# Optimization experiments

Measured on AMD Instinct MI355X. Metric: run time of the kernel, lower is better.

The kernel has to match this reference:

```python
import jax, jax.numpy as jnp
import numpy as np

N_NODES = 65536
N_EDGES = 524288
N_GRAPHS = 512
G_NODES = 10000
NUM_DISEASES = 2000
IN_DIM = 128
HID = 256  # 2 * IN_DIM (z_emb concat feat)
D_FEAT = 512
C_FEAT = 512
MAX_Z = 4000


def setup_inputs() -> dict:
    key = jax.random.key(0)
    ks = jax.random.split(key, 20)
    rn = lambda k, shape: jax.random.normal(k, shape, dtype=jnp.float32) * 0.05
    return {
        "z": jax.random.randint(ks[0], (N_NODES,), 0, MAX_Z),
        "node_id": jnp.sort(jax.random.randint(ks[1], (N_NODES,), 0, G_NODES)),
        "src": jax.random.randint(ks[2], (N_EDGES,), 0, N_NODES),
        "dst": jax.random.randint(ks[3], (N_EDGES,), 0, N_NODES),
        "graph_ids": jnp.sort(jax.random.randint(ks[4], (N_NODES,), 0, N_GRAPHS)),
        "z_table": rn(ks[5], (MAX_Z, IN_DIM)),
        "d_feat_tab": rn(ks[6], (G_NODES, D_FEAT)),
        "c_feat_tab": rn(ks[7], (G_NODES, C_FEAT)),
        "Wd": rn(ks[8], (D_FEAT, IN_DIM)),
        "Wc": rn(ks[9], (C_FEAT, IN_DIM)),
        "gin_W1": rn(ks[10], (HID, HID)), "gin_b1": jnp.zeros((HID,), jnp.float32),
        "gin_W2": rn(ks[11], (HID, HID)), "gin_b2": jnp.zeros((HID,), jnp.float32),
        "sage_Wself": rn(ks[12], (HID, HID)),
        "sage_Wneigh": rn(ks[13], (HID, HID)),
        "sage_b": jnp.zeros((HID,), jnp.float32),
        "lin1_W": rn(ks[14], (HID, HID)), "lin1_b": jnp.zeros((HID,), jnp.float32),
        "lin2_W": rn(ks[15], (HID, 1)), "lin2_b": jnp.zeros((1,), jnp.float32),
    }


def reference(z, node_id, src, dst, graph_ids, z_table, d_feat_tab, c_feat_tab,
              Wd, Wc, gin_W1, gin_b1, gin_W2, gin_b2,
              sage_Wself, sage_Wneigh, sage_b, lin1_W, lin1_b, lin2_W, lin2_b):
    # --- input feature construction (Model.forward) ---
    z_emb = z_table[z]                               # [N, IN_DIM]
    d_proj = d_feat_tab[node_id] @ Wd                # d_fc (bias=False)
    c_proj = c_feat_tab[node_id] @ Wc                # c_fc (bias=False)
    disease = (node_id <= NUM_DISEASES)[:, None]
    # node_id is sorted -> masked concat order == node order
    feat = jnp.where(disease, d_proj, c_proj)        # [N, IN_DIM]
    x = jnp.concatenate([z_emb, feat], axis=1)       # [N, HID]
    # --- GINConv: sum aggregation, eps=0, mlp = Lin->ReLU->Lin ---
    agg = jax.ops.segment_sum(x[src], dst, num_segments=N_NODES)
    h = x + agg
    h = jax.nn.relu(h @ gin_W1 + gin_b1) @ gin_W2 + gin_b2
    # --- SAGEConv('mean'): fc_self(h) + fc_neigh(mean_neighbors) + bias ---
    deg = jax.ops.segment_sum(jnp.ones((N_EDGES,), h.dtype), dst, num_segments=N_NODES)
    mean_n = jax.ops.segment_sum(h[src], dst, num_segments=N_NODES) / jnp.maximum(deg, 1.0)[:, None]
    h = h @ sage_Wself + mean_n @ sage_Wneigh + sage_b
    # --- per-graph max pooling readout ---
    g = jax.ops.segment_max(h, graph_ids, num_segments=N_GRAPHS, indices_are_sorted=True)
    g = jnp.where(jnp.isfinite(g), g, 0.0)           # guard empty graphs
    # --- head: Linear -> ReLU -> (dropout p=0, eval) -> Linear ---
    h = jax.nn.relu(g @ lin1_W + lin1_b)
    return h @ lin2_W + lin2_b                       # [N_GRAPHS, 1]
```

## Files before the change

### kernel.cpp

```cpp
#include <hip/hip_runtime.h>
#include <hip/hip_bf16.h>

#define N_NODES     65536
#define N_EDGES     524288
#define N_GRAPHS    512
#define G_NODES_N   10000
#define NUM_DIS     2000
#define IN_DIM      128
#define HID         256
#define D_FEAT      512
#define MAX_Z       4000
#define POOL_SPLIT  8

typedef _Float16 half8 __attribute__((ext_vector_type(8)));
typedef float    f32x4 __attribute__((ext_vector_type(4)));

typedef __attribute__((address_space(1))) const void as1_void;
typedef __attribute__((address_space(3))) void       as3_void;

__global__ __launch_bounds__(256) void prep_kernel(
    const float* __restrict__ Ws, const float* __restrict__ Wn,
    const float* __restrict__ Wd, const float* __restrict__ Wc,
    const float* __restrict__ W1, const float* __restrict__ W2,
    const float* __restrict__ z_table,
    const int* __restrict__ z, const int* __restrict__ node_id,
    _Float16* __restrict__ WsT, _Float16* __restrict__ WnT,
    _Float16* __restrict__ WdT, _Float16* __restrict__ WcT,
    _Float16* __restrict__ W12P, _Float16* __restrict__ zt16,
    int2* __restrict__ zn2, int* __restrict__ cnt, int* __restrict__ flags)
{
    const int b = blockIdx.x;
    const int tid = threadIdx.x;
    if (b < 64) {
        __shared__ float tile[64][65];
        const float* W; _Float16* T; int K, N, k0, n0;
        if (b < 32) {
            const int mat = b >> 4, t = b & 15;
            K = HID; N = HID; k0 = (t >> 2) * 64; n0 = (t & 3) * 64;
            W = (mat == 0) ? Ws : Wn;
            T = (mat == 0) ? WsT : WnT;
        } else {
            const int bb = b - 32;
            const int mat = bb >> 4, t = bb & 15;
            K = D_FEAT; N = IN_DIM; k0 = (t >> 1) * 64; n0 = (t & 1) * 64;
            W = (mat == 0) ? Wd : Wc;
            T = (mat == 0) ? WdT : WcT;
        }
        const int tx = tid & 63, ty = tid >> 6;
        #pragma unroll
        for (int r = 0; r < 64; r += 4)
            tile[r + ty][tx] = W[(size_t)(k0 + r + ty) * N + n0 + tx];
        __syncthreads();
        #pragma unroll
        for (int c = 0; c < 64; c += 4)
            T[(size_t)(n0 + c + ty) * K + k0 + tx] = (_Float16)tile[tx][c + ty];
    } else if (b < 576) {
        const int bb = b - 64;
        const int mat = bb >> 8;
        const int k = bb & 255;
        const int n = tid;
        const float* W = mat ? W2 : W1;
        const float v = W[(size_t)k * HID + n];
        const size_t idx = (size_t)(mat * 8 + (k >> 5)) * 8192
                         + (size_t)((((k >> 3) & 3) * 256 + n) * 8 + (k & 7));
        W12P[idx] = (_Float16)v;
    } else if (b < 826) {
        const size_t base = ((size_t)(b - 576) * 256 + tid) * 8;
        const float4 f0 = *(const float4*)(z_table + base);
        const float4 f1 = *(const float4*)(z_table + base + 4);
        half8 h;
        h[0]=(_Float16)f0.x; h[1]=(_Float16)f0.y; h[2]=(_Float16)f0.z; h[3]=(_Float16)f0.w;
        h[4]=(_Float16)f1.x; h[5]=(_Float16)f1.y; h[6]=(_Float16)f1.z; h[7]=(_Float16)f1.w;
        *(half8*)(zt16 + base) = h;
    } else if (b < 890) {
        const int base = (b - 826) * 1024 + tid * 4;
        *(int4*)(cnt + base) = make_int4(0, 0, 0, 0);
        if (b == 826 && tid < 128) flags[tid] = 0;
    } else {
        const int i = (b - 890) * 256 + tid;
        zn2[i] = make_int2(z[i], node_id[i]);
    }
}

__global__ __launch_bounds__(256) void proj_mfma_kernel(
    const float* __restrict__ dtab, const float* __restrict__ ctab,
    const _Float16* __restrict__ WdT, const _Float16* __restrict__ WcT,
    _Float16* __restrict__ proj)
{
    __shared__ _Float16 Alds[128 * 40];
    __shared__ _Float16 Blds[128 * 40];
    const int blk = blockIdx.x;
    const float* tab; const _Float16* WT; int base, M, bm;
    if (blk < 16) { tab = dtab; WT = WdT; base = 0;           M = NUM_DIS + 1;             bm = blk * 128; }
    else          { tab = ctab; WT = WcT; base = NUM_DIS + 1; M = G_NODES_N - NUM_DIS - 1; bm = (blk - 16) * 128; }
    const int tid  = threadIdx.x;
    const int wave = tid >> 6, lane = tid & 63;
    const int q    = lane >> 4, l16 = lane & 15;
    const int mbase = (wave & 1) * 64, nbase = (wave >> 1) * 64;
    const int r = tid >> 1, s = tid & 1;

    f32x4 acc[4][4] = {};

    for (int kc = 0; kc < 16; ++kc) {
        const int k0 = kc * 32;
        const int arow = min(bm + r, M - 1);
        const float* gA = tab + (size_t)(base + arow) * D_FEAT + k0 + s * 16;
        const _Float16* gB = WT + (size_t)r * D_FEAT + k0 + s * 16;
        const float4 f0 = ((const float4*)gA)[0];
        const float4 f1 = ((const float4*)gA)[1];
        const float4 f2 = ((const float4*)gA)[2];
        const float4 f3 = ((const float4*)gA)[3];
        const half8 hb0 = *(const half8*)gB;
        const half8 hb1 = *(const half8*)(gB + 8);
        half8 h0, h1;
        h0[0]=(_Float16)f0.x; h0[1]=(_Float16)f0.y; h0[2]=(_Float16)f0.z; h0[3]=(_Float16)f0.w;
        h0[4]=(_Float16)f1.x; h0[5]=(_Float16)f1.y; h0[6]=(_Float16)f1.z; h0[7]=(_Float16)f1.w;
        h1[0]=(_Float16)f2.x; h1[1]=(_Float16)f2.y; h1[2]=(_Float16)f2.z; h1[3]=(_Float16)f2.w;
        h1[4]=(_Float16)f3.x; h1[5]=(_Float16)f3.y; h1[6]=(_Float16)f3.z; h1[7]=(_Float16)f3.w;
        __syncthreads();
        *(half8*)&Alds[r * 40 + s * 16]     = h0;
        *(half8*)&Alds[r * 40 + s * 16 + 8] = h1;
        *(half8*)&Blds[r * 40 + s * 16]     = hb0;
        *(half8*)&Blds[r * 40 + s * 16 + 8] = hb1;
        __syncthreads();
        half8 a[4], b[4];
        #pragma unroll
        for (int i = 0; i < 4; ++i)
            a[i] = *(const half8*)&Alds[(mbase + i * 16 + l16) * 40 + q * 8];
        #pragma unroll
        for (int j = 0; j < 4; ++j)
            b[j] = *(const half8*)&Blds[(nbase + j * 16 + l16) * 40 + q * 8];
        #pragma unroll
        for (int i = 0; i < 4; ++i)
            #pragma unroll
            for (int j = 0; j < 4; ++j)
                acc[i][j] = __builtin_amdgcn_mfma_f32_16x16x32_f16(a[i], b[j], acc[i][j], 0, 0, 0);
    }

    #pragma unroll
    for (int j = 0; j < 4; ++j) {
        const int colg = nbase + j * 16 + l16;
        #pragma unroll
        for (int i = 0; i < 4; ++i) {
            #pragma unroll
            for (int rr = 0; rr < 4; ++rr) {
                const int row = bm + mbase + i * 16 + q * 4 + rr;
                if (row < M)
                    proj[(size_t)(base + row) * IN_DIM + colg] = (_Float16)acc[i][j][rr];
            }
        }
    }
}

__global__ __launch_bounds__(256) void hist_kernel(
    const int* __restrict__ dst, int* __restrict__ cnt)
{
    const int e = blockIdx.x * 256 + threadIdx.x;
    if (e < N_EDGES) atomicAdd(&cnt[dst[e]], 1);
}

__global__ __launch_bounds__(256) void scan_fused_kernel(
    const int* __restrict__ cnt, int* __restrict__ row_ptr,
    int* __restrict__ fill, int* __restrict__ flags)
{
    __shared__ int a[256], b[256];
    __shared__ int sums[64];
    __shared__ int segbase;
    const int t = threadIdx.x;
    const int blk = blockIdx.x;
    const int base = blk * 1024 + t * 4;
    const int4 c = *(const int4*)(cnt + base);
    const int s = c.x + c.y + c.z + c.w;
    a[t] = s;
    __syncthreads();
    int* in = a; int* out = b;
    for (int off = 1; off < 256; off <<= 1) {
        out[t] = in[t] + ((t >= off) ? in[t - off] : 0);
        __syncthreads();
        int* tmp = in; in = out; out = tmp;
    }
    if (t == 0) {
        atomicExch(&flags[64 + blk], in[255]);
        __threadfence();
        atomicAdd(&flags[0], 1);
        while (atomicAdd(&flags[0], 0) < 64) {}
    }
    __syncthreads();
    if (t < 64) sums[t] = atomicAdd(&flags[64 + t], 0);
    __syncthreads();
    if (t == 0) {
        int pfx = 0;
        for (int i = 0; i < blk; ++i) pfx += sums[i];
        segbase = pfx;
        if (blk == 63) {
            int tot = pfx;
            for (int i = blk; i < 64; ++i) tot += sums[i];
            row_ptr[N_NODES] = tot;
        }
    }
    __syncthreads();
    const int run = in[t] - s + segbase;
    int4 r;
    r.x = run; r.y = run + c.x; r.z = r.y + c.y; r.w = r.z + c.z;
    *(int4*)(row_ptr + base) = r;
    *(int4*)(fill + base) = r;
}

__global__ __launch_bounds__(256) void scatter_kernel(
    const int* __restrict__ src, const int* __restrict__ dst,
    const int2* __restrict__ zn2,
    int* __restrict__ fill, int* __restrict__ col, int2* __restrict__ colzn)
{
    const int e = blockIdx.x * 256 + threadIdx.x;
    if (e < N_EDGES) {
        const int s = src[e];
        const int pos = atomicAdd(&fill[dst[e]], 1);
        col[pos] = s;
        colzn[pos] = zn2[s];
    }
}

__global__ __launch_bounds__(256) void gin_fused_kernel(
    const int* __restrict__ row_ptr, const int2* __restrict__ colzn,
    const int2* __restrict__ zn2,
    const _Float16* __restrict__ zt16, const _Float16* __restrict__ proj,
    const _Float16* __restrict__ W12P,
    const float* __restrict__ b1, const float* __restrict__ b2,
    _Float16* __restrict__ H)
{
    __shared__ _Float16 Apanel[32 * 264];
    __shared__ _Float16 Blds[2][8192];

    const int bm   = blockIdx.x * 32;
    const int tid  = threadIdx.x;
    const int wave = tid >> 6, lane = tid & 63;
    const int q    = lane >> 4, l16 = lane & 15;
    const int nbase = wave * 64;

    auto stage = [&](int c, int buf) {
        const _Float16* src = W12P + (size_t)c * 8192;
        #pragma unroll
        for (int tt = 0; tt < 4; ++tt) {
            const int seg = (wave * 4 + tt) * 64 + lane;
            __builtin_amdgcn_global_load_lds((as1_void*)(src + seg * 8),
                (as3_void*)&Blds[buf][(wave * 4 + tt) * 64 * 8], 16, 0, 0);
        }
    };

    stage(0, 0);

    {
        const int r = tid >> 3, p = tid & 7;
        const int gr = bm + r;
        const int beg = row_ptr[gr], end = row_ptr[gr + 1];
        float za[16], pa[16];
        {
            const int2 zn = zn2[gr];
            const half8* zp = (const half8*)(zt16 + (size_t)zn.x * IN_DIM + p * 16);
            const half8* pp = (const half8*)(proj + (size_t)zn.y * IN_DIM + p * 16);
            const half8 z0 = zp[0], z1 = zp[1], p0 = pp[0], p1 = pp[1];
            #pragma unroll
            for (int i = 0; i < 8; ++i) {
                za[i] = (float)z0[i]; za[8 + i] = (float)z1[i];
                pa[i] = (float)p0[i]; pa[8 + i] = (float)p1[i];
            }
        }
        int e = beg;
        for (; e + 2 <= end; e += 2) {
            const int2 znA = colzn[e];
            const int2 znB = colzn[e + 1];
            const half8* zpA = (const half8*)(zt16 + (size_t)znA.x * IN_DIM + p * 16);
            const half8* ppA = (const half8*)(proj + (size_t)znA.y * IN_DIM + p * 16);
            const half8* zpB = (const half8*)(zt16 + (size_t)znB.x * IN_DIM + p * 16);
            const half8* ppB = (const half8*)(proj + (size_t)znB.y * IN_DIM + p * 16);
            const half8 zA0 = zpA[0], zA1 = zpA[1], pA0 = ppA[0], pA1 = ppA[1];
            const half8 zB0 = zpB[0], zB1 = zpB[1], pB0 = ppB[0], pB1 = ppB[1];
            #pragma unroll
            for (int i = 0; i < 8; ++i) {
                za[i]     += (float)zA0[i] + (float)zB0[i];
                za[8 + i] += (float)zA1[i] + (float)zB1[i];
                pa[i]     += (float)pA0[i] + (float)pB0[i];
                pa[8 + i] += (float)pA1[i] + (float)pB1[i];
            }
        }
        if (e < end) {
            const int2 zn = colzn[e];
            const half8* zp = (const half8*)(zt16 + (size_t)zn.x * IN_DIM + p * 16);
            const half8* pp = (const half8*)(proj + (size_t)zn.y * IN_DIM + p * 16);
            const half8 z0 = zp[0], z1 = zp[1], p0 = pp[0], p1 = pp[1];
            #pragma unroll
            for (int i = 0; i < 8; ++i) {
                za[i] += (float)z0[i]; za[8 + i] += (float)z1[i];
                pa[i] += (float)p0[i]; pa[8 + i] += (float)p1[i];
            }
        }
        half8 oz0, oz1, op0, op1;
        #pragma unroll
        for (int i = 0; i < 8; ++i) {
            oz0[i] = (_Float16)za[i];     oz1[i] = (_Float16)za[8 + i];
            op0[i] = (_Float16)pa[i];     op1[i] = (_Float16)pa[8 + i];
        }
        *(half8*)&Apanel[r * 264 + p * 16]           = oz0;
        *(half8*)&Apanel[r * 264 + p * 16 + 8]       = oz1;
        *(half8*)&Apanel[r * 264 + 128 + p * 16]     = op0;
        *(half8*)&Apanel[r * 264 + 128 + p * 16 + 8] = op1;
    }
    __syncthreads();

    f32x4 acc[2][4] = {};
    int pb = 0;
    for (int c = 0; c < 16; ++c) {
        if (c + 1 < 16) stage(c + 1, pb ^ 1);
        if (c == 8) {
            #pragma unroll
            for (int j = 0; j < 4; ++j) {
                const int colg = nbase + j * 16 + l16;
                const float bv = b1[colg];
                #pragma unroll
                for (int i = 0; i < 2; ++i)
                    #pragma unroll
                    for (int rr = 0; rr < 4; ++rr) {
                        const float v = fmaxf(acc[i][j][rr] + bv, 0.0f);
                        Apanel[(i * 16 + q * 4 + rr) * 264 + colg] = (_Float16)v;
                        acc[i][j][rr] = 0.0f;
                    }
            }
            __syncthreads();
        }
        const int kl = (c & 7) * 32;
        half8 a[2], b[4];
        #pragma unroll
        for (int i = 0; i < 2; ++i)
            a[i] = *(const half8*)&Apanel[(i * 16 + l16) * 264 + kl + q * 8];
        #pragma unroll
        for (int j = 0; j < 4; ++j)
            b[j] = *(const half8*)&Blds[pb][(q * 256 + nbase + j * 16 + l16) * 8];
        #pragma unroll
        for (int i = 0; i < 2; ++i)
            #pragma unroll
            for (int j = 0; j < 4; ++j)
                acc[i][j] = __builtin_amdgcn_mfma_f32_16x16x32_f16(a[i], b[j], acc[i][j], 0, 0, 0);
        __syncthreads();
        pb ^= 1;
    }

    #pragma unroll
    for (int j = 0; j < 4; ++j) {
        const int colg = nbase + j * 16 + l16;
        const float bv = b2[colg];
        #pragma unroll
        for (int i = 0; i < 2; ++i)
            #pragma unroll
            for (int rr = 0; rr < 4; ++rr) {
                const int rowg = bm + i * 16 + q * 4 + rr;
                H[(size_t)rowg * HID + colg] = (_Float16)(acc[i][j][rr] + bv);
            }
    }
}

__global__ __launch_bounds__(256) void csr_agg_kernel(
    const int* __restrict__ row_ptr, const int* __restrict__ col,
    const _Float16* __restrict__ F, _Float16* __restrict__ OUT)
{
    const int t = blockIdx.x * 256 + threadIdx.x;
    const int d = t >> 5;
    const int q = t & 31;
    const int beg = row_ptr[d];
    const int end = row_ptr[d + 1];
    float acc[8] = {0.f,0.f,0.f,0.f,0.f,0.f,0.f,0.f};
    int e = beg;
    for (; e + 4 <= end; e += 4) {
        const int s0 = col[e],     s1 = col[e + 1];
        const int s2 = col[e + 2], s3 = col[e + 3];
        const half8 v0 = *(const half8*)(F + (size_t)s0 * HID + q * 8);
        const half8 v1 = *(const half8*)(F + (size_t)s1 * HID + q * 8);
        const half8 v2 = *(const half8*)(F + (size_t)s2 * HID + q * 8);
        const half8 v3 = *(const half8*)(F + (size_t)s3 * HID + q * 8);
        #pragma unroll
        for (int i = 0; i < 8; ++i)
            acc[i] += ((float)v0[i] + (float)v1[i]) + ((float)v2[i] + (float)v3[i]);
    }
    for (; e < end; ++e) {
        const half8 v0 = *(const half8*)(F + (size_t)col[e] * HID + q * 8);
        #pragma unroll
        for (int i = 0; i < 8; ++i) acc[i] += (float)v0[i];
    }
    const float rs = 1.0f / fmaxf((float)(end - beg), 1.0f);
    half8 o;
    #pragma unroll
    for (int i = 0; i < 8; ++i) o[i] = (_Float16)(acc[i] * rs);
    *(half8*)(OUT + (size_t)d * HID + q * 8) = o;
}

__global__ __launch_bounds__(256) void mfma_gemm_kernel(
    const _Float16* __restrict__ A1, const _Float16* __restrict__ A2,
    const _Float16* __restrict__ B1T, const _Float16* __restrict__ B2T,
    const float* __restrict__ bias, _Float16* __restrict__ Ch)
{
    __shared__ _Float16 Alds[128 * 32];
    __shared__ _Float16 Blds[128 * 32];
    const int bm   = blockIdx.x * 128;
    const int bn   = blockIdx.y * 128;
    const int tid  = threadIdx.x;
    const int wave = tid >> 6, lane = tid & 63;
    const int q    = lane >> 4, l16 = lane & 15;
    const int mbase = (wave & 1) * 64, nbase = (wave >> 1) * 64;

    f32x4 acc[4][4] = {};

    for (int kc = 0; kc < 16; ++kc) {
        const int k0 = (kc & 7) * 32;
        const _Float16* Abase = (kc < 8) ? A1 : A2;
        const _Float16* Bbase = (kc < 8) ? B1T : B2T;
        __syncthreads();
        #pragma unroll
        for (int t = 0; t < 2; ++t) {
            const int i   = wave * 128 + t * 64 + lane;
            const int row = i >> 2, s = i & 3;
            const _Float16* gA = Abase + (size_t)(bm + row) * HID + k0 + s * 8;
            const _Float16* gB = Bbase + (size_t)(bn + row) * HID + k0 + s * 8;
            __builtin_amdgcn_global_load_lds(
                (as1_void*)gA, (as3_void*)&Alds[(wave * 128 + t * 64) * 8], 16, 0, 0);
            __builtin_amdgcn_global_load_lds(
                (as1_void*)gB, (as3_void*)&Blds[(wave * 128 + t * 64) * 8], 16, 0, 0);
        }
        __syncthreads();
        half8 a[4], b[4];
        #pragma unroll
        for (int i = 0; i < 4; ++i)
            a[i] = *(const half8*)&Alds[(mbase + i * 16 + l16) * 32 + q * 8];
        #pragma unroll
        for (int j = 0; j < 4; ++j)
            b[j] = *(const half8*)&Blds[(nbase + j * 16 + l16) * 32 + q * 8];
        #pragma unroll
        for (int i = 0; i < 4; ++i)
            #pragma unroll
            for (int j = 0; j < 4; ++j)
                acc[i][j] = __builtin_amdgcn_mfma_f32_16x16x32_f16(a[i], b[j], acc[i][j], 0, 0, 0);
    }

    #pragma unroll
    for (int j = 0; j < 4; ++j) {
        const int colg = bn + nbase + j * 16 + l16;
        const float bv = bias[colg];
        #pragma unroll
        for (int i = 0; i < 4; ++i) {
            #pragma unroll
            for (int rr = 0; rr < 4; ++rr) {
                const int rowg = bm + mbase + i * 16 + q * 4 + rr;
                Ch[(size_t)rowg * HID + colg] = (_Float16)(acc[i][j][rr] + bv);
            }
        }
    }
}

__global__ __launch_bounds__(256) void pool_part_kernel(
    const _Float16* __restrict__ H2, const int* __restrict__ gid,
    float* __restrict__ Gpart)
{
    const int g = blockIdx.y;
    const int sp = blockIdx.x;
    const int j = threadIdx.x;
    int lo = 0, hi = N_NODES;
    while (lo < hi) { const int mid = (lo + hi) >> 1; if (gid[mid] < g) lo = mid + 1; else hi = mid; }
    const int start = lo;
    hi = N_NODES;
    while (lo < hi) { const int mid = (lo + hi) >> 1; if (gid[mid] < g + 1) lo = mid + 1; else hi = mid; }
    const int end = lo;
    float m = -INFINITY;
    for (int i = start + sp; i < end; i += POOL_SPLIT)
        m = fmaxf(m, (float)H2[(size_t)i * HID + j]);
    Gpart[((size_t)g * POOL_SPLIT + sp) * HID + j] = m;
}

__global__ __launch_bounds__(256) void head_kernel(
    const float* __restrict__ Gpart,
    const float* __restrict__ W1, const float* __restrict__ b1,
    const float* __restrict__ W2, const float* __restrict__ b2,
    float* __restrict__ out)
{
    const int g = blockIdx.x;
    const int j = threadIdx.x;
    __shared__ float row[HID];
    __shared__ float red[HID];
    float m = -INFINITY;
    #pragma unroll
    for (int sp = 0; sp < POOL_SPLIT; ++sp)
        m = fmaxf(m, Gpart[((size_t)g * POOL_SPLIT + sp) * HID + j]);
    row[j] = (m == -INFINITY) ? 0.0f : m;
    __syncthreads();
    float acc = b1[j];
    #pragma unroll 8
    for (int k = 0; k < HID; ++k)
        acc = fmaf(row[k], W1[k * HID + j], acc);
    acc = fmaxf(acc, 0.f);
    red[j] = acc * W2[j];
    __syncthreads();
    for (int s = 128; s > 0; s >>= 1) {
        if (j < s) red[j] += red[j + s];
        __syncthreads();
    }
    if (j == 0) out[g] = red[0] + b2[0];
}

extern "C" void kernel_launch(void* const* d_in, const int* in_sizes, int n_in,
                              void* d_out, int out_size, void* d_ws, size_t ws_size,
                              hipStream_t stream)
{
    const int*   z         = (const int*)d_in[0];
    const int*   node_id   = (const int*)d_in[1];
    const int*   src       = (const int*)d_in[2];
    const int*   dst       = (const int*)d_in[3];
    const int*   graph_ids = (const int*)d_in[4];
    const float* z_table   = (const float*)d_in[5];
    const float* d_feat    = (const float*)d_in[6];
    const float* c_feat    = (const float*)d_in[7];
    const float* Wd        = (const float*)d_in[8];
    const float* Wc        = (const float*)d_in[9];
    const float* gin_W1    = (const float*)d_in[10];
    const float* gin_b1    = (const float*)d_in[11];
    const float* gin_W2    = (const float*)d_in[12];
    const float* gin_b2    = (const float*)d_in[13];
    const float* sage_Wself  = (const float*)d_in[14];
    const float* sage_Wneigh = (const float*)d_in[15];
    const float* sage_b    = (const float*)d_in[16];
    const float* lin1_W    = (const float*)d_in[17];
    const float* lin1_b    = (const float*)d_in[18];
    const float* lin2_W    = (const float*)d_in[19];
    const float* lin2_b    = (const float*)d_in[20];
    float* out = (float*)d_out;

    const size_t NH = (size_t)N_NODES * HID;
    char* wsb = (char*)d_ws;
    _Float16* Hh   = (_Float16*)wsb;                     wsb += NH * 2;
    _Float16* AGGh = (_Float16*)wsb;                     wsb += NH * 2;
    _Float16* H2h  = (_Float16*)wsb;                     wsb += NH * 2;
    _Float16* projh= (_Float16*)wsb;                     wsb += (size_t)G_NODES_N * IN_DIM * 2;
    _Float16* W12P = (_Float16*)wsb;                     wsb += 16 * 8192 * 2;
    _Float16* WsT  = (_Float16*)wsb;                     wsb += HID * HID * 2;
    _Float16* WnT  = (_Float16*)wsb;                     wsb += HID * HID * 2;
    _Float16* WdT  = (_Float16*)wsb;                     wsb += D_FEAT * IN_DIM * 2;
    _Float16* WcT  = (_Float16*)wsb;                     wsb += D_FEAT * IN_DIM * 2;
    _Float16* zt16 = (_Float16*)wsb;                     wsb += (size_t)MAX_Z * IN_DIM * 2;
    int2* zn2      = (int2*)wsb;                         wsb += (size_t)N_NODES * 8;
    int2* colzn    = (int2*)wsb;                         wsb += (size_t)N_EDGES * 8;
    float* Gpart   = (float*)wsb;                        wsb += (size_t)N_GRAPHS * POOL_SPLIT * HID * 4;
    int* row_ptr   = (int*)wsb;                          wsb += (N_NODES + 4) * 4;
    int* cnt       = (int*)wsb;                          wsb += N_NODES * 4;
    int* fill      = (int*)wsb;                          wsb += N_NODES * 4;
    int* col       = (int*)wsb;                          wsb += N_EDGES * 4;
    int* flags     = (int*)wsb;                          wsb += 128 * 4;

    prep_kernel<<<1146, 256, 0, stream>>>(
        sage_Wself, sage_Wneigh, Wd, Wc, gin_W1, gin_W2, z_table, z, node_id,
        WsT, WnT, WdT, WcT, W12P, zt16, zn2, cnt, flags);

    hist_kernel<<<N_EDGES / 256, 256, 0, stream>>>(dst, cnt);
    scan_fused_kernel<<<64, 256, 0, stream>>>(cnt, row_ptr, fill, flags);
    scatter_kernel<<<N_EDGES / 256, 256, 0, stream>>>(src, dst, zn2, fill, col, colzn);

    proj_mfma_kernel<<<16 + 63, 256, 0, stream>>>(d_feat, c_feat, WdT, WcT, projh);

    gin_fused_kernel<<<N_NODES / 32, 256, 0, stream>>>(
        row_ptr, colzn, zn2, zt16, projh, W12P, gin_b1, gin_b2, Hh);

    csr_agg_kernel<<<(N_NODES * 32) / 256, 256, 0, stream>>>(row_ptr, col, Hh, AGGh);

    dim3 ggrid(N_NODES / 128, HID / 128);
    mfma_gemm_kernel<<<ggrid, 256, 0, stream>>>(Hh, AGGh, WsT, WnT, sage_b, H2h);

    dim3 pgrid(POOL_SPLIT, N_GRAPHS);
    pool_part_kernel<<<pgrid, 256, 0, stream>>>(H2h, graph_ids, Gpart);
    head_kernel<<<N_GRAPHS, 256, 0, stream>>>(Gpart, lin1_W, lin1_b, lin2_W, lin2_b, out);
}
```

Measured before the change: 374.4 us.

## Fuse projection with histogram, enlarge GIN row tile, deepen gather unrolling

The projection GEMM and the degree histogram now run as one launch, with extra blocks doing the atomics, which removes a launch and lets the two overlap. The fused GIN kernel now handles 64 rows per block in two gather passes, with a 4x4 MFMA accumulator tile and a single-buffered weight stage. It also unrolls the edge gather by four. The CSR aggregation adds an 8-way unrolled gather loop to keep more loads in flight. The trade-offs are more LDS and registers per block (lower occupancy) and losing the double-buffered weight prefetch, which adds extra barriers per chunk.

```diff
diff --git a/kernel.cpp b/kernel.cpp
--- a/kernel.cpp
+++ b/kernel.cpp
@@ -82,14 +82,20 @@
     }
 }
 
-__global__ __launch_bounds__(256) void proj_mfma_kernel(
+__global__ __launch_bounds__(256) void proj_hist_kernel(
     const float* __restrict__ dtab, const float* __restrict__ ctab,
     const _Float16* __restrict__ WdT, const _Float16* __restrict__ WcT,
-    _Float16* __restrict__ proj)
-{
+    _Float16* __restrict__ proj,
+    const int* __restrict__ dst, int* __restrict__ cnt)
+{
+    const int blk = blockIdx.x;
+    if (blk >= 79) {
+        const int e = (blk - 79) * 256 + threadIdx.x;
+        if (e < N_EDGES) atomicAdd(&cnt[dst[e]], 1);
+        return;
+    }
     __shared__ _Float16 Alds[128 * 40];
     __shared__ _Float16 Blds[128 * 40];
-    const int blk = blockIdx.x;
     const float* tab; const _Float16* WT; int base, M, bm;
     if (blk < 16) { tab = dtab; WT = WdT; base = 0;           M = NUM_DIS + 1;             bm = blk * 128; }
     else          { tab = ctab; WT = WcT; base = NUM_DIS + 1; M = G_NODES_N - NUM_DIS - 1; bm = (blk - 16) * 128; }
@@ -152,13 +158,6 @@
     }
 }
 
-__global__ __launch_bounds__(256) void hist_kernel(
-    const int* __restrict__ dst, int* __restrict__ cnt)
-{
-    const int e = blockIdx.x * 256 + threadIdx.x;
-    if (e < N_EDGES) atomicAdd(&cnt[dst[e]], 1);
-}
-
 __global__ __launch_bounds__(256) void scan_fused_kernel(
     const int* __restrict__ cnt, int* __restrict__ row_ptr,
     int* __restrict__ fill, int* __restrict__ flags)
@@ -228,120 +227,147 @@
     const float* __restrict__ b1, const float* __restrict__ b2,
     _Float16* __restrict__ H)
 {
-    __shared__ _Float16 Apanel[32 * 264];
-    __shared__ _Float16 Blds[2][8192];
-
-    const int bm   = blockIdx.x * 32;
+    __shared__ _Float16 Apanel[64 * 264];
+    __shared__ _Float16 Blds[8192];
+
+    const int bm   = blockIdx.x * 64;
     const int tid  = threadIdx.x;
     const int wave = tid >> 6, lane = tid & 63;
     const int q    = lane >> 4, l16 = lane & 15;
     const int nbase = wave * 64;
 
-    auto stage = [&](int c, int buf) {
+    auto stage = [&](int c) {
         const _Float16* src = W12P + (size_t)c * 8192;
         #pragma unroll
         for (int tt = 0; tt < 4; ++tt) {
             const int seg = (wave * 4 + tt) * 64 + lane;
             __builtin_amdgcn_global_load_lds((as1_void*)(src + seg * 8),
-                (as3_void*)&Blds[buf][(wave * 4 + tt) * 64 * 8], 16, 0, 0);
+                (as3_void*)&Blds[(wave * 4 + tt) * 64 * 8], 16, 0, 0);
         }
     };
 
-    stage(0, 0);
+    stage(0);
 
     {
-        const int r = tid >> 3, p = tid & 7;
-        const int gr = bm + r;
-        const int beg = row_ptr[gr], end = row_ptr[gr + 1];
-        float za[16], pa[16];
-        {
-            const int2 zn = zn2[gr];
-            const half8* zp = (const half8*)(zt16 + (size_t)zn.x * IN_DIM + p * 16);
-            const half8* pp = (const half8*)(proj + (size_t)zn.y * IN_DIM + p * 16);
-            const half8 z0 = zp[0], z1 = zp[1], p0 = pp[0], p1 = pp[1];
+        const int p = tid & 7;
+        #pragma unroll 1
+        for (int pass = 0; pass < 2; ++pass) {
+            const int r  = (tid >> 3) + (pass << 5);
+            const int gr = bm + r;
+            const int beg = row_ptr[gr], end = row_ptr[gr + 1];
+            float za[16], pa[16];
+            {
+                const int2 zn = zn2[gr];
+                const half8* zp = (const half8*)(zt16 + (size_t)zn.x * IN_DIM + p * 16);
+                const half8* pp = (const half8*)(proj + (size_t)zn.y * IN_DIM + p * 16);
+                const half8 z0 = zp[0], z1 = zp[1], p0 = pp[0], p1 = pp[1];
+                #pragma unroll
+                for (int i = 0; i < 8; ++i) {
+                    za[i] = (float)z0[i]; za[8 + i] = (float)z1[i];
+                    pa[i] = (float)p0[i]; pa[8 + i] = (float)p1[i];
+                }
+            }
+            int e = beg;
+            for (; e + 4 <= end; e += 4) {
+                const int2 znA = colzn[e],     znB = colzn[e + 1];
+                const int2 znC = colzn[e + 2], znD = colzn[e + 3];
+                const half8* zpA = (const half8*)(zt16 + (size_t)znA.x * IN_DIM + p * 16);
+                const half8* ppA = (const half8*)(proj + (size_t)znA.y * IN_DIM + p * 16);
+                const half8* zpB = (const half8*)(zt16 + (size_t)znB.x * IN_DIM + p * 16);
+                const half8* ppB = (const half8*)(proj + (size_t)znB.y * IN_DIM + p * 16);
+                const half8* zpC = (const half8*)(zt16 + (size_t)znC.x * IN_DIM + p * 16);
+                const half8* ppC = (const half8*)(proj + (size_t)znC.y * IN_DIM + p * 16);
+                const half8* zpD = (const half8*)(zt16 + (size_t)znD.x * IN_DIM + p * 16);
+                const half8* ppD = (const half8*)(proj + (size_t)znD.y * IN_DIM + p * 16);
+                const half8 zA0 = zpA[0], zA1 = zpA[1], pA0 = ppA[0], pA1 = ppA[1];
+                const half8 zB0 = zpB[0], zB1 = zpB[1], pB0 = ppB[0], pB1 = ppB[1];
+                const half8 zC0 = zpC[0], zC1 = zpC[1], pC0 = ppC[0], pC1 = ppC[1];
+                const half8 zD0 = zpD[0], zD1 = zpD[1], pD0 = ppD[0], pD1 = ppD[1];
+                #pragma unroll
+                for (int i = 0; i < 8; ++i) {
+                    za[i]     += ((float)zA0[i] + (float)zB0[i]) + ((float)zC0[i] + (float)zD0[i]);
+                    za[8 + i] += ((float)zA1[i] + (float)zB1[i]) + ((float)zC1[i] + (float)zD1[i]);
+                    pa[i]     += ((float)pA0[i] + (float)pB0[i]) + ((float)pC0[i] + (float)pD0[i]);
+                    pa[8 + i] += ((float)pA1[i] + (float)pB1[i]) + ((float)pC1[i] + (float)pD1[i]);
+                }
+            }
+            for (; e + 2 <= end; e += 2) {
+                const int2 znA = colzn[e];
+                const int2 znB = colzn[e + 1];
+                const half8* zpA = (const half8*)(zt16 + (size_t)znA.x * IN_DIM + p * 16);
+                const half8* ppA = (const half8*)(proj + (size_t)znA.y * IN_DIM + p * 16);
+                const half8* zpB = (const half8*)(zt16 + (size_t)znB.x * IN_DIM + p * 16);
+                const half8* ppB = (const half8*)(proj + (size_t)znB.y * IN_DIM + p * 16);
+                const half8 zA0 = zpA[0], zA1 = zpA[1], pA0 = ppA[0], pA1 = ppA[1];
+                const half8 zB0 = zpB[0], zB1 = zpB[1], pB0 = ppB[0], pB1 = ppB[1];
+                #pragma unroll
+                for (int i = 0; i < 8; ++i) {
+                    za[i]     += (float)zA0[i] + (float)zB0[i];
+                    za[8 + i] += (float)zA1[i] + (float)zB1[i];
+                    pa[i]     += (float)pA0[i] + (float)pB0[i];
+                    pa[8 + i] += (float)pA1[i] + (float)pB1[i];
+                }
+            }
+            if (e < end) {
+                const int2 zn = colzn[e];
+                const half8* zp = (const half8*)(zt16 + (size_t)zn.x * IN_DIM + p * 16);
+                const half8* pp = (const half8*)(proj + (size_t)zn.y * IN_DIM + p * 16);
+                const half8 z0 = zp[0], z1 = zp[1], p0 = pp[0], p1 = pp[1];
+                #pragma unroll
+                for (int i = 0; i < 8; ++i) {
+                    za[i] += (float)z0[i]; za[8 + i] += (float)z1[i];
+                    pa[i] += (float)p0[i]; pa[8 + i] += (float)p1[i];
+                }
+            }
+            half8 oz0, oz1, op0, op1;
             #pragma unroll
             for (int i = 0; i < 8; ++i) {
-                za[i] = (float)z0[i]; za[8 + i] = (float)z1[i];
-                pa[i] = (float)p0[i]; pa[8 + i] = (float)p1[i];
-            }
-        }
-        int e = beg;
-        for (; e + 2 <= end; e += 2) {
-            const int2 znA = colzn[e];
-            const int2 znB = colzn[e + 1];
-            const half8* zpA = (const half8*)(zt16 + (size_t)znA.x * IN_DIM + p * 16);
-            const half8* ppA = (const half8*)(proj + (size_t)znA.y * IN_DIM + p * 16);
-            const half8* zpB = (const half8*)(zt16 + (size_t)znB.x * IN_DIM + p * 16);
-            const half8* ppB = (const half8*)(proj + (size_t)znB.y * IN_DIM + p * 16);
-            const half8 zA0 = zpA[0], zA1 = zpA[1], pA0 = ppA[0], pA1 = ppA[1];
-            const half8 zB0 = zpB[0], zB1 = zpB[1], pB0 = ppB[0], pB1 = ppB[1];
-            #pragma unroll
-            for (int i = 0; i < 8; ++i) {
-                za[i]     += (float)zA0[i] + (float)zB0[i];
-                za[8 + i] += (float)zA1[i] + (float)zB1[i];
-                pa[i]     += (float)pA0[i] + (float)pB0[i];
-                pa[8 + i] += (float)pA1[i] + (float)pB1[i];
-            }
-        }
-        if (e < end) {
-            const int2 zn = colzn[e];
-            const half8* zp = (const half8*)(zt16 + (size_t)zn.x * IN_DIM + p * 16);
-            const half8* pp = (const half8*)(proj + (size_t)zn.y * IN_DIM + p * 16);
-            const half8 z0 = zp[0], z1 = zp[1], p0 = pp[0], p1 = pp[1];
-            #pragma unroll
-            for (int i = 0; i < 8; ++i) {
-                za[i] += (float)z0[i]; za[8 + i] += (float)z1[i];
-                pa[i] += (float)p0[i]; pa[8 + i] += (float)p1[i];
-            }
-        }
-        half8 oz0, oz1, op0, op1;
-        #pragma unroll
-        for (int i = 0; i < 8; ++i) {
-            oz0[i] = (_Float16)za[i];     oz1[i] = (_Float16)za[8 + i];
-            op0[i] = (_Float16)pa[i];     op1[i] = (_Float16)pa[8 + i];
-        }
-        *(half8*)&Apanel[r * 264 + p * 16]           = oz0;
-        *(half8*)&Apanel[r * 264 + p * 16 + 8]       = oz1;
-        *(half8*)&Apanel[r * 264 + 128 + p * 16]     = op0;
-        *(half8*)&Apanel[r * 264 + 128 + p * 16 + 8] = op1;
+                oz0[i] = (_Float16)za[i];     oz1[i] = (_Float16)za[8 + i];
+                op0[i] = (_Float16)pa[i];     op1[i] = (_Float16)pa[8 + i];
+            }
+            *(half8*)&Apanel[r * 264 + p * 16]           = oz0;
+            *(half8*)&Apanel[r * 264 + p * 16 + 8]       = oz1;
+            *(half8*)&Apanel[r * 264 + 128 + p * 16]     = op0;
+            *(half8*)&Apanel[r * 264 + 128 + p * 16 + 8] = op1;
+        }
     }
     __syncthreads();
 
-    f32x4 acc[2][4] = {};
-    int pb = 0;
+    f32x4 acc[4][4] = {};
     for (int c = 0; c < 16; ++c) {
-        if (c + 1 < 16) stage(c + 1, pb ^ 1);
-        if (c == 8) {
-            #pragma unroll
-            for (int j = 0; j < 4; ++j) {
-                const int colg = nbase + j * 16 + l16;
-                const float bv = b1[colg];
+        if (c) {
+            __syncthreads();
+            stage(c);
+            if (c == 8) {
                 #pragma unroll
-                for (int i = 0; i < 2; ++i)
+                for (int j = 0; j < 4; ++j) {
+                    const int colg = nbase + j * 16 + l16;
+                    const float bv = b1[colg];
                     #pragma unroll
-                    for (int rr = 0; rr < 4; ++rr) {
-                        const float v = fmaxf(acc[i][j][rr] + bv, 0.0f);
-                        Apanel[(i * 16 + q * 4 + rr) * 264 + colg] = (_Float16)v;
-                        acc[i][j][rr] = 0.0f;
-                    }
+                    for (int i = 0; i < 4; ++i)
+                        #pragma unroll
+                        for (int rr = 0; rr < 4; ++rr) {
+                            const float v = fmaxf(acc[i][j][rr] + bv, 0.0f);
+                            Apanel[(i * 16 + q * 4 + rr) * 264 + colg] = (_Float16)v;
+                            acc[i][j][rr] = 0.0f;
+                        }
+                }
             }
             __syncthreads();
         }
         const int kl = (c & 7) * 32;
-        half8 a[2], b[4];
-        #pragma unroll
-        for (int i = 0; i < 2; ++i)
+        half8 a[4], b[4];
+        #pragma unroll
+        for (int i = 0; i < 4; ++i)
             a[i] = *(const half8*)&Apanel[(i * 16 + l16) * 264 + kl + q * 8];
         #pragma unroll
         for (int j = 0; j < 4; ++j)
-            b[j] = *(const half8*)&Blds[pb][(q * 256 + nbase + j * 16 + l16) * 8];
-        #pragma unroll
-        for (int i = 0; i < 2; ++i)
+            b[j] = *(const half8*)&Blds[(q * 256 + nbase + j * 16 + l16) * 8];
+        #pragma unroll
+        for (int i = 0; i < 4; ++i)
             #pragma unroll
             for (int j = 0; j < 4; ++j)
                 acc[i][j] = __builtin_amdgcn_mfma_f32_16x16x32_f16(a[i], b[j], acc[i][j], 0, 0, 0);
-        __syncthreads();
-        pb ^= 1;
     }
 
     #pragma unroll
@@ -349,7 +375,7 @@
         const int colg = nbase + j * 16 + l16;
         const float bv = b2[colg];
         #pragma unroll
-        for (int i = 0; i < 2; ++i)
+        for (int i = 0; i < 4; ++i)
             #pragma unroll
             for (int rr = 0; rr < 4; ++rr) {
                 const int rowg = bm + i * 16 + q * 4 + rr;
@@ -369,6 +395,24 @@
     const int end = row_ptr[d + 1];
     float acc[8] = {0.f,0.f,0.f,0.f,0.f,0.f,0.f,0.f};
     int e = beg;
+    for (; e + 8 <= end; e += 8) {
+        const int s0 = col[e],     s1 = col[e + 1];
+        const int s2 = col[e + 2], s3 = col[e + 3];
+        const int s4 = col[e + 4], s5 = col[e + 5];
+        const int s6 = col[e + 6], s7 = col[e + 7];
+        const half8 v0 = *(const half8*)(F + (size_t)s0 * HID + q * 8);
+        const half8 v1 = *(const half8*)(F + (size_t)s1 * HID + q * 8);
+        const half8 v2 = *(const half8*)(F + (size_t)s2 * HID + q * 8);
+        const half8 v3 = *(const half8*)(F + (size_t)s3 * HID + q * 8);
+        const half8 v4 = *(const half8*)(F + (size_t)s4 * HID + q * 8);
+        const half8 v5 = *(const half8*)(F + (size_t)s5 * HID + q * 8);
+        const half8 v6 = *(const half8*)(F + (size_t)s6 * HID + q * 8);
+        const half8 v7 = *(const half8*)(F + (size_t)s7 * HID + q * 8);
+        #pragma unroll
+        for (int i = 0; i < 8; ++i)
+            acc[i] += (((float)v0[i] + (float)v1[i]) + ((float)v2[i] + (float)v3[i]))
+                    + (((float)v4[i] + (float)v5[i]) + ((float)v6[i] + (float)v7[i]));
+    }
     for (; e + 4 <= end; e += 4) {
         const int s0 = col[e],     s1 = col[e + 1];
         const int s2 = col[e + 2], s3 = col[e + 3];
@@ -555,13 +599,13 @@
         sage_Wself, sage_Wneigh, Wd, Wc, gin_W1, gin_W2, z_table, z, node_id,
         WsT, WnT, WdT, WcT, W12P, zt16, zn2, cnt, flags);
 
-    hist_kernel<<<N_EDGES / 256, 256, 0, stream>>>(dst, cnt);
+    proj_hist_kernel<<<79 + N_EDGES / 256, 256, 0, stream>>>(
+        d_feat, c_feat, WdT, WcT, projh, dst, cnt);
+
     scan_fused_kernel<<<64, 256, 0, stream>>>(cnt, row_ptr, fill, flags);
     scatter_kernel<<<N_EDGES / 256, 256, 0, stream>>>(src, dst, zn2, fill, col, colzn);
 
-    proj_mfma_kernel<<<16 + 63, 256, 0, stream>>>(d_feat, c_feat, WdT, WcT, projh);
-
-    gin_fused_kernel<<<N_NODES / 32, 256, 0, stream>>>(
+    gin_fused_kernel<<<N_NODES / 64, 256, 0, stream>>>(
         row_ptr, colzn, zn2, zt16, projh, W12P, gin_b1, gin_b2, Hh);
 
     csr_agg_kernel<<<(N_NODES * 32) / 256, 256, 0, stream>>>(row_ptr, col, Hh, AGGh);
```

New measurement: 360.6 us. 1.04x faster.
